# Kernel tuning notes

Hardware: AMD Instinct MI355X
Metric: run time of the kernel (lower is better)

The kernel has to match this reference:

```python
import jax, jax.numpy as jnp
import numpy as np

B, N, C, H, KHOP = 8, 1024, 512, 16, 2
HD = C // H
VALID = 768          # valid (non-padded) nodes per batch row
E = B * VALID * 32   # ~deg 32 per valid node
BN_EPS = 1e-5
LN_EPS = 1e-5


def setup_inputs() -> dict:
    key = jax.random.key(0)
    ks = jax.random.split(key, 12)
    x = jax.random.normal(ks[0], (B, N, C), jnp.float32)
    shift = jax.random.normal(ks[1], (B, C), jnp.float32) * 0.1
    scale = jax.random.normal(ks[2], (B, C), jnp.float32) * 0.1
    # fixed-size valid prefix per row -> static shapes under jit
    mask = jnp.broadcast_to(jnp.arange(N) < VALID, (B, N))
    # edges live inside a single graph (same batch row), only among valid nodes,
    # expressed directly in flattened [B*N] index space (== compacted indexing up to relabeling)
    eb = jax.random.randint(ks[3], (E,), 0, B)
    es = jax.random.randint(ks[4], (E,), 0, VALID)
    ed = jax.random.randint(ks[5], (E,), 0, VALID)
    edge_index = jnp.stack([eb * N + es, eb * N + ed]).astype(jnp.int32)
    w = lambda k, s: jax.random.normal(k, s, jnp.float32) * 0.02
    gin_eps = jnp.zeros((KHOP,), jnp.float32)
    gin_w1 = w(ks[6], (KHOP, C, 2 * C)); gin_b1 = jnp.zeros((KHOP, 2 * C), jnp.float32)
    gin_bn_g = jnp.ones((KHOP, 2 * C), jnp.float32); gin_bn_b = jnp.zeros((KHOP, 2 * C), jnp.float32)
    gin_w2 = w(ks[7], (KHOP, 2 * C, C)); gin_b2 = jnp.zeros((KHOP, C), jnp.float32)
    ln_g = jnp.ones((C,), jnp.float32); ln_b = jnp.zeros((C,), jnp.float32)
    qkv_w = w(ks[8], (C, 3 * C)); qkv_b = jnp.zeros((3 * C,), jnp.float32)
    proj_w = w(ks[9], (C, C)); proj_b = jnp.zeros((C,), jnp.float32)
    return dict(x=x, shift=shift, scale=scale, mask=mask, edge_index=edge_index,
                gin_eps=gin_eps, gin_w1=gin_w1, gin_b1=gin_b1, gin_bn_g=gin_bn_g,
                gin_bn_b=gin_bn_b, gin_w2=gin_w2, gin_b2=gin_b2, ln_g=ln_g, ln_b=ln_b,
                qkv_w=qkv_w, qkv_b=qkv_b, proj_w=proj_w, proj_b=proj_b)


def _gin_layer(h, mask_f, cnt, src, dst, eps, w1, b1, g, bt, w2, b2):
    # GINConv: mlp((1+eps)*x_i + sum_{j->i} x_j); MLP = Linear->BatchNorm(batch stats over valid nodes)->ReLU->Linear
    agg = jax.ops.segment_sum(h[src], dst, num_segments=B * N)  # scatter-add messages
    z = (1.0 + eps) * h + agg
    pre = z @ w1 + b1                              # [B*N, 2C]
    mw = mask_f[:, None]
    mean = (pre * mw).sum(0) / cnt                 # masked BN statistics (valid nodes only)
    var = (((pre - mean) ** 2) * mw).sum(0) / cnt  # biased var, as torch BatchNorm
    hn = jax.nn.relu(g * (pre - mean) * jax.lax.rsqrt(var + BN_EPS) + bt)
    return (hn @ w2 + b2) * mw                     # zero out padded nodes (x_struct stays 0 there)


def reference(x, shift, scale, mask, edge_index, gin_eps, gin_w1, gin_b1, gin_bn_g,
              gin_bn_b, gin_w2, gin_b2, ln_g, ln_b, qkv_w, qkv_b, proj_w, proj_b):
    xf = x.reshape(B * N, C)
    mask_f = mask.reshape(-1).astype(x.dtype)
    cnt = mask_f.sum()
    src, dst = edge_index[0], edge_index[1]
    # structure extractor: k-hop GIN with residual after the first hop
    h = _gin_layer(xf * mask_f[:, None], mask_f, cnt, src, dst, gin_eps[0],
                   gin_w1[0], gin_b1[0], gin_bn_g[0], gin_bn_b[0], gin_w2[0], gin_b2[0])
    for i in range(1, KHOP):
        h = _gin_layer(h, mask_f, cnt, src, dst, gin_eps[i],
                       gin_w1[i], gin_b1[i], gin_bn_g[i], gin_bn_b[i], gin_w2[i], gin_b2[i]) + h
    xs = x + h.reshape(B, N, C)  # x + x_struct (x_struct zero on padded nodes)
    # LayerNorm + modulate
    mu = xs.mean(-1, keepdims=True)
    va = xs.var(-1, keepdims=True)
    xn = (xs - mu) * jax.lax.rsqrt(va + LN_EPS) * ln_g + ln_b
    xm = xn * (1.0 + scale[:, None, :]) + shift[:, None, :]
    # SDPA attention with key padding mask
    qkv = (xm @ qkv_w + qkv_b).reshape(B, N, 3, H, HD).transpose(2, 0, 3, 1, 4)
    q, k, v = qkv[0], qkv[1], qkv[2]                       # [B,H,N,HD]
    scores = jnp.einsum('bhqd,bhkd->bhqk', q, k) * (HD ** -0.5)
    scores = scores + jnp.where(mask[:, None, None, :], 0.0, -1e9)
    attn = jax.nn.softmax(scores, axis=-1)
    out = jnp.einsum('bhqk,bhkd->bhqd', attn, v).transpose(0, 2, 1, 3).reshape(B, N, C)
    return out @ proj_w + proj_b
```

## Files before the change

### kernel.cpp

```cpp
#include <hip/hip_runtime.h>
#include <hip/hip_bf16.h>

constexpr int Bc    = 8;
constexpr int Nn    = 1024;
constexpr int Cc    = 512;
constexpr int Hh    = 16;
constexpr int HD    = 32;
constexpr int VALID = 768;
constexpr float CNT_INV = 1.0f / 6144.0f;
constexpr float BN_EPS = 1e-5f;
constexpr float LN_EPS = 1e-5f;
constexpr int ROWS = Bc * Nn;
constexpr int VROWS = Bc * VALID;

typedef short s16x8 __attribute__((ext_vector_type(8)));
typedef float f32x4 __attribute__((ext_vector_type(4)));

static __device__ __forceinline__ unsigned short f2bf(float f) {
    __hip_bfloat16 h = __float2bfloat16(f);
    return *reinterpret_cast<unsigned short*>(&h);
}
static __device__ __forceinline__ float bf2f(unsigned short u) {
    unsigned int v = (unsigned int)u << 16;
    union { unsigned int u; float f; } c; c.u = v;
    return c.f;
}

static __device__ __forceinline__ int vswz(int d) {
    return ((((d >> 3) ^ (d >> 1)) & 3) << 1) | (d & 1);
}

__global__ __launch_bounds__(256) void k_wt_all(const float* __restrict__ gw1,
                                                const float* __restrict__ gw2,
                                                const float* __restrict__ qkvw,
                                                const float* __restrict__ projw,
                                                const float* __restrict__ x,
                                                unsigned short* __restrict__ w1t,
                                                unsigned short* __restrict__ w2t,
                                                unsigned short* __restrict__ qkvt,
                                                unsigned short* __restrict__ projt,
                                                unsigned short* __restrict__ xb,
                                                float* __restrict__ stats,
                                                int* __restrict__ ideg) {
    const int bi = blockIdx.x;
    if (bi >= 3072) {
        int e = (bi - 3072) * 2048 + threadIdx.x * 8;
        float4 a = *(const float4*)&x[e];
        float4 b = *(const float4*)&x[e + 4];
        s16x8 o;
        o[0] = (short)f2bf(a.x); o[1] = (short)f2bf(a.y);
        o[2] = (short)f2bf(a.z); o[3] = (short)f2bf(a.w);
        o[4] = (short)f2bf(b.x); o[5] = (short)f2bf(b.y);
        o[6] = (short)f2bf(b.z); o[7] = (short)f2bf(b.w);
        *(s16x8*)&xb[e] = o;
        return;
    }
    if (bi == 0) {
        for (int i = threadIdx.x; i < 4096; i += 256) stats[i] = 0.f;
    } else if (bi == 1) {
        for (int i = threadIdx.x; i < 8192; i += 256) ideg[i] = 0;
    }

    const float* W; unsigned short* Wt; int K, N, bx, by;
    if (bi < 1024) {
        int z = bi >> 9, r = bi & 511;
        W = gw1 + (size_t)z * 524288; Wt = w1t + (size_t)z * 524288;
        K = 512; N = 1024; bx = r & 31; by = r >> 5;
    } else if (bi < 2048) {
        int z = (bi - 1024) >> 9, r = (bi - 1024) & 511;
        W = gw2 + (size_t)z * 524288; Wt = w2t + (size_t)z * 524288;
        K = 1024; N = 512; bx = r & 15; by = r >> 4;
    } else if (bi < 2816) {
        int r = bi - 2048;
        W = qkvw; Wt = qkvt; K = 512; N = 1536; bx = r % 48; by = r / 48;
    } else {
        int r = bi - 2816;
        W = projw; Wt = projt; K = 512; N = 512; bx = r & 15; by = r >> 4;
    }

    __shared__ float t[32][33];
    const int k0 = by * 32, n0 = bx * 32;
    int kk = threadIdx.x >> 3, nn = (threadIdx.x & 7) * 4;
    float4 v = *(const float4*)&W[(size_t)(k0 + kk) * N + n0 + nn];
    t[kk][nn] = v.x; t[kk][nn + 1] = v.y; t[kk][nn + 2] = v.z; t[kk][nn + 3] = v.w;
    __syncthreads();
    int nn2 = threadIdx.x >> 3, kk2 = (threadIdx.x & 7) * 4;
    ushort4 o;
    o.x = f2bf(t[kk2][nn2]);     o.y = f2bf(t[kk2 + 1][nn2]);
    o.z = f2bf(t[kk2 + 2][nn2]); o.w = f2bf(t[kk2 + 3][nn2]);
    *(ushort4*)&Wt[(size_t)(n0 + nn2) * K + k0 + kk2] = o;
}

__global__ __launch_bounds__(256) void k_count(const int* __restrict__ ei,
                                               int* __restrict__ deg, int E) {
    int e = blockIdx.x * 256 + threadIdx.x;
    if (e < E) atomicAdd(&deg[ei[E + e]], 1);
}

__global__ __launch_bounds__(1024) void k_scan(const int* __restrict__ deg,
                                               int* __restrict__ start,
                                               int* __restrict__ cursor) {
    __shared__ int csum[1024];
    const int t = threadIdx.x;
    const int base = t * 8;
    int local[8];
    int s = 0;
#pragma unroll
    for (int i = 0; i < 8; ++i) { local[i] = deg[base + i]; s += local[i]; }
    csum[t] = s;
    __syncthreads();
    for (int off = 1; off < 1024; off <<= 1) {
        int v = (t >= off) ? csum[t - off] : 0;
        __syncthreads();
        if (t >= off) csum[t] += v;
        __syncthreads();
    }
    int excl = (t == 0) ? 0 : csum[t - 1];
#pragma unroll
    for (int i = 0; i < 8; ++i) {
        start[base + i]  = excl;
        cursor[base + i] = excl;
        excl += local[i];
    }
    if (t == 1023) start[8192] = excl;
}

__global__ __launch_bounds__(256) void k_fill(const int* __restrict__ ei,
                                              int* __restrict__ cursor,
                                              int* __restrict__ list, int E) {
    int e = blockIdx.x * 256 + threadIdx.x;
    if (e < E) {
        int pos = atomicAdd(&cursor[ei[E + e]], 1);
        list[pos] = ei[e];
    }
}

__global__ __launch_bounds__(128) void k_gather_z(const unsigned short* __restrict__ h,
                                                  const int* __restrict__ start,
                                                  const int* __restrict__ list,
                                                  const float* __restrict__ epsArr,
                                                  int layer,
                                                  unsigned short* __restrict__ z) {
    const int vr = blockIdx.x;
    const int batch = vr / 768;
    const int row = batch * 1024 + (vr - batch * 768);
    const int c = threadIdx.x * 4;
    const int s0 = start[row], s1 = start[row + 1];
    const float e1 = 1.0f + epsArr[layer];
    const unsigned short* hp = h + c;
    ushort4 bv = *(const ushort4*)&h[(size_t)row * 512 + c];
    float a0 = bf2f(bv.x) * e1, a1 = bf2f(bv.y) * e1;
    float a2 = bf2f(bv.z) * e1, a3 = bf2f(bv.w) * e1;
    int j = s0;
    for (; j + 4 <= s1; j += 4) {
        int sA = list[j], sB = list[j + 1], sC = list[j + 2], sD = list[j + 3];
        ushort4 vA = *(const ushort4*)&hp[(size_t)sA * 512];
        ushort4 vB = *(const ushort4*)&hp[(size_t)sB * 512];
        ushort4 vC = *(const ushort4*)&hp[(size_t)sC * 512];
        ushort4 vD = *(const ushort4*)&hp[(size_t)sD * 512];
        a0 += bf2f(vA.x); a1 += bf2f(vA.y); a2 += bf2f(vA.z); a3 += bf2f(vA.w);
        a0 += bf2f(vB.x); a1 += bf2f(vB.y); a2 += bf2f(vB.z); a3 += bf2f(vB.w);
        a0 += bf2f(vC.x); a1 += bf2f(vC.y); a2 += bf2f(vC.z); a3 += bf2f(vC.w);
        a0 += bf2f(vD.x); a1 += bf2f(vD.y); a2 += bf2f(vD.z); a3 += bf2f(vD.w);
    }
    for (; j < s1; ++j) {
        int sA = list[j];
        ushort4 vA = *(const ushort4*)&hp[(size_t)sA * 512];
        a0 += bf2f(vA.x); a1 += bf2f(vA.y); a2 += bf2f(vA.z); a3 += bf2f(vA.w);
    }
    ushort4 o;
    o.x = f2bf(a0); o.y = f2bf(a1); o.z = f2bf(a2); o.w = f2bf(a3);
    *(ushort4*)&z[(size_t)row * 512 + c] = o;
}

template <bool RESIDUAL, bool STATS, bool SKIPM, bool OUTBF, bool QSCALE, bool HBF>
__global__ __launch_bounds__(256) void k_gemm_bf(const unsigned short* __restrict__ A,
                                                 const unsigned short* __restrict__ Bt,
                                                 const float* __restrict__ bias,
                                                 const float* __restrict__ res,
                                                 void* __restrict__ Cd,
                                                 float* __restrict__ stats,
                                                 unsigned short* __restrict__ hb,
                                                 int K, int Nc) {
    __shared__ unsigned short Al[128 * 64];
    __shared__ unsigned short Bl[128 * 64];
    const int tid  = threadIdx.x;
    const int by   = blockIdx.y;
    const int bm   = SKIPM ? ((by / 6) * 1024 + (by % 6) * 128) : (by * 128);
    const int bn   = blockIdx.x * 128;
    const int wid  = tid >> 6, lane = tid & 63;
    const int wr   = wid >> 1, wc = wid & 1;
    const int lo16 = lane & 15, g = lane >> 4;

    const int sr = tid >> 1;
    const int sh = tid & 1;
    const size_t a_off = (size_t)(bm + sr) * K + sh * 32;
    const size_t b_off = (size_t)(bn + sr) * K + sh * 32;

    f32x4 acc[4][4];
#pragma unroll
    for (int m = 0; m < 4; ++m)
#pragma unroll
        for (int n = 0; n < 4; ++n) acc[m][n] = (f32x4){0.f, 0.f, 0.f, 0.f};

    const int NT = K >> 6;
    s16x8 ar[4], br[4];
    {
        const s16x8* ap = (const s16x8*)(A + a_off);
        const s16x8* bp = (const s16x8*)(Bt + b_off);
#pragma unroll
        for (int i = 0; i < 4; ++i) { ar[i] = ap[i]; br[i] = bp[i]; }
    }

    for (int kt = 0; kt < NT; ++kt) {
        __syncthreads();
#pragma unroll
        for (int i = 0; i < 4; ++i) {
            int sl = (sh * 4 + i) ^ (sr & 7);
            *(s16x8*)&Al[sr * 64 + sl * 8] = ar[i];
            *(s16x8*)&Bl[sr * 64 + sl * 8] = br[i];
        }
        __syncthreads();
        if (kt + 1 < NT) {
            const s16x8* ap = (const s16x8*)(A + a_off + (size_t)(kt + 1) * 64);
            const s16x8* bp = (const s16x8*)(Bt + b_off + (size_t)(kt + 1) * 64);
#pragma unroll
            for (int i = 0; i < 4; ++i) { ar[i] = ap[i]; br[i] = bp[i]; }
        }
#pragma unroll
        for (int ks = 0; ks < 2; ++ks) {
            s16x8 af[4], bfr[4];
#pragma unroll
            for (int m = 0; m < 4; ++m) {
                int r = wr * 64 + m * 16 + lo16;
                int sl = (ks * 4 + g) ^ (r & 7);
                af[m] = *(const s16x8*)&Al[r * 64 + sl * 8];
            }
#pragma unroll
            for (int n = 0; n < 4; ++n) {
                int r = wc * 64 + n * 16 + lo16;
                int sl = (ks * 4 + g) ^ (r & 7);
                bfr[n] = *(const s16x8*)&Bl[r * 64 + sl * 8];
            }
            __builtin_amdgcn_s_setprio(1);
#pragma unroll
            for (int m = 0; m < 4; ++m)
#pragma unroll
                for (int n = 0; n < 4; ++n)
                    acc[m][n] = __builtin_amdgcn_mfma_f32_16x16x32_bf16(
                        af[m], bfr[n], acc[m][n], 0, 0, 0);
            __builtin_amdgcn_s_setprio(0);
        }
    }

#pragma unroll
    for (int n = 0; n < 4; ++n) {
        int col = bn + wc * 64 + n * 16 + lo16;
        float bb = bias[col];
        bool qs = QSCALE && (col < 512);
        float s = 0.f, s2 = 0.f;
#pragma unroll
        for (int m = 0; m < 4; ++m) {
#pragma unroll
            for (int ri = 0; ri < 4; ++ri) {
                int row = bm + wr * 64 + m * 16 + g * 4 + ri;
                float v = acc[m][n][ri] + bb;
                if (STATS) { s += v; s2 += v * v; }
                if (RESIDUAL) v += res[(size_t)row * Nc + col];
                if (QSCALE && qs) v *= 0.17677669529663687f;
                if (OUTBF) ((unsigned short*)Cd)[(size_t)row * Nc + col] = f2bf(v);
                else       ((float*)Cd)[(size_t)row * Nc + col] = v;
                if (HBF)   hb[(size_t)row * Nc + col] = f2bf(v);
            }
        }
        if (STATS) {
            s  += __shfl_xor(s, 16);  s  += __shfl_xor(s, 32);
            s2 += __shfl_xor(s2, 16); s2 += __shfl_xor(s2, 32);
            if (g == 0) {
                atomicAdd(&stats[col], s);
                atomicAdd(&stats[1024 + col], s2);
            }
        }
    }
}

__global__ __launch_bounds__(256) void k_bn_apply(const float* __restrict__ pre,
                                                  const float* __restrict__ stats,
                                                  const float* __restrict__ g,
                                                  const float* __restrict__ bt,
                                                  unsigned short* __restrict__ hn) {
    const int vr = blockIdx.x;
    const int batch = vr / 768;
    const int row = batch * 1024 + (vr - batch * 768);
    const int c0 = threadIdx.x * 4;
    const size_t off = (size_t)row * 1024 + c0;
    float4 v  = *(const float4*)&pre[off];
    float4 sm = *(const float4*)&stats[c0];
    float4 sq = *(const float4*)&stats[1024 + c0];
    float4 gv = *(const float4*)&g[c0];
    float4 bv = *(const float4*)&bt[c0];

    float m0 = sm.x * CNT_INV, m1 = sm.y * CNT_INV, m2 = sm.z * CNT_INV, m3 = sm.w * CNT_INV;
    float r0 = rsqrtf(sq.x * CNT_INV - m0 * m0 + BN_EPS);
    float r1 = rsqrtf(sq.y * CNT_INV - m1 * m1 + BN_EPS);
    float r2 = rsqrtf(sq.z * CNT_INV - m2 * m2 + BN_EPS);
    float r3 = rsqrtf(sq.w * CNT_INV - m3 * m3 + BN_EPS);
    ushort4 o;
    o.x = f2bf(fmaxf(gv.x * (v.x - m0) * r0 + bv.x, 0.f));
    o.y = f2bf(fmaxf(gv.y * (v.y - m1) * r1 + bv.y, 0.f));
    o.z = f2bf(fmaxf(gv.z * (v.z - m2) * r2 + bv.z, 0.f));
    o.w = f2bf(fmaxf(gv.w * (v.w - m3) * r3 + bv.w, 0.f));
    *(ushort4*)&hn[off] = o;
}

__global__ __launch_bounds__(256) void k_ln_mod(const float* __restrict__ x,
                                                const float* __restrict__ h,
                                                const float* __restrict__ lg,
                                                const float* __restrict__ lb,
                                                const float* __restrict__ sc,
                                                const float* __restrict__ sh,
                                                unsigned short* __restrict__ xm) {
    int row  = blockIdx.x * 4 + (threadIdx.x >> 6);
    int lane = threadIdx.x & 63;
    const size_t base = (size_t)row * 512 + lane * 8;
    const bool val = (row & 1023) < VALID;

    float v[8];
    float4 a0 = *(const float4*)&x[base],     a1 = *(const float4*)&x[base + 4];
    float4 b0 = *(const float4*)&h[base],     b1 = *(const float4*)&h[base + 4];
    if (!val) { b0.x=b0.y=b0.z=b0.w=0.f; b1.x=b1.y=b1.z=b1.w=0.f; }
    v[0] = a0.x + b0.x; v[1] = a0.y + b0.y; v[2] = a0.z + b0.z; v[3] = a0.w + b0.w;
    v[4] = a1.x + b1.x; v[5] = a1.y + b1.y; v[6] = a1.z + b1.z; v[7] = a1.w + b1.w;

    float s = 0.f, s2 = 0.f;
#pragma unroll
    for (int j = 0; j < 8; ++j) { s += v[j]; s2 += v[j] * v[j]; }
#pragma unroll
    for (int off = 32; off; off >>= 1) {
        s  += __shfl_xor(s, off);
        s2 += __shfl_xor(s2, off);
    }
    float mu  = s * (1.0f / 512.0f);
    float var = s2 * (1.0f / 512.0f) - mu * mu;
    float rs  = rsqrtf(var + LN_EPS);

    int c0 = lane * 8;
    int bidx = row >> 10;
    const float* scp = sc + (size_t)bidx * 512 + c0;
    const float* shp = sh + (size_t)bidx * 512 + c0;
    s16x8 o;
#pragma unroll
    for (int j = 0; j < 8; ++j) {
        float xn = (v[j] - mu) * rs * lg[c0 + j] + lb[c0 + j];
        o[j] = (short)f2bf(xn * (1.0f + scp[j]) + shp[j]);
    }
    *(s16x8*)&xm[base] = o;
}

__global__ __launch_bounds__(256) void k_attn_mfma(const unsigned short* __restrict__ qkv,
                                                   unsigned short* __restrict__ att) {
    __shared__ __align__(16) unsigned short Kl[128 * 32];
    __shared__ __align__(16) unsigned short Vt[32 * 128];
    __shared__ __align__(16) unsigned short Pl[4][16 * 128];

    const int w    = threadIdx.x >> 6;
    const int lane = threadIdx.x & 63;
    const int bh   = blockIdx.x;
    const int b    = bh >> 4, h = bh & 15;
    const int qt   = blockIdx.y;
    const int lo16 = lane & 15;
    const int g    = lane >> 4;

    const int qrow = qt * 64 + w * 16 + lo16;
    s16x8 qf = *(const s16x8*)&qkv[(size_t)(b * 1024 + qrow) * 1536 + h * 32 + g * 8];

    f32x4 o0 = {0.f, 0.f, 0.f, 0.f}, o1 = {0.f, 0.f, 0.f, 0.f};
    float l_run = 0.f;

    const size_t kvbase = (size_t)(b * 1024) * 1536 + h * 32;

    const int kr_r = threadIdx.x >> 2;
    const int kr_g = threadIdx.x & 3;
    const int vk0  = (threadIdx.x >> 2) * 2;
    const int vgg  = threadIdx.x & 3;

    s16x8 kA, kB, vA, vB;
    {
        const unsigned short* kp = &qkv[kvbase + (size_t)kr_r * 1536 + 512 + kr_g * 8];
        kA = *(const s16x8*)kp;
        kB = *(const s16x8*)(kp + (size_t)64 * 1536);
        const unsigned short* vp = &qkv[kvbase + (size_t)vk0 * 1536 + 1024 + vgg * 8];
        vA = *(const s16x8*)vp;
        vB = *(const s16x8*)(vp + 1536);
    }

    for (int kc = 0; kc < VALID; kc += 128) {
        __syncthreads();

        {
            int slot = kr_g ^ ((kr_r >> 1) & 3);
            *(s16x8*)&Kl[kr_r * 32 + slot * 8] = kA;
            int r2 = 64 + kr_r;
            slot = kr_g ^ ((r2 >> 1) & 3);
            *(s16x8*)&Kl[r2 * 32 + slot * 8] = kB;
        }
#pragma unroll
        for (int j = 0; j < 8; ++j) {
            int d = vgg * 8 + j;
            int slot = (vk0 >> 3) ^ vswz(d);
            int elem = d * 128 + slot * 8 + (vk0 & 7);
            unsigned int pack = (unsigned int)(unsigned short)vA[j] |
                                ((unsigned int)(unsigned short)vB[j] << 16);
            *(unsigned int*)&Vt[elem] = pack;
        }
        __syncthreads();

        if (kc + 128 < VALID) {
            const unsigned short* kp = &qkv[kvbase + (size_t)(kc + 128 + kr_r) * 1536 + 512 + kr_g * 8];
            kA = *(const s16x8*)kp;
            kB = *(const s16x8*)(kp + (size_t)64 * 1536);
            const unsigned short* vp = &qkv[kvbase + (size_t)(kc + 128 + vk0) * 1536 + 1024 + vgg * 8];
            vA = *(const s16x8*)vp;
            vB = *(const s16x8*)(vp + 1536);
        }

        f32x4 sc[8];
        __builtin_amdgcn_s_setprio(1);
#pragma unroll
        for (int t = 0; t < 8; ++t) {
            int r = t * 16 + lo16;
            int slot = g ^ ((r >> 1) & 3);
            s16x8 kf = *(const s16x8*)&Kl[r * 32 + slot * 8];
            f32x4 z = {0.f, 0.f, 0.f, 0.f};
            sc[t] = __builtin_amdgcn_mfma_f32_16x16x32_bf16(kf, qf, z, 0, 0, 0);
        }
        __builtin_amdgcn_s_setprio(0);

        float lsum = 0.f;
#pragma unroll
        for (int t = 0; t < 8; ++t) {
            float p0 = __expf(sc[t][0]);
            float p1 = __expf(sc[t][1]);
            float p2 = __expf(sc[t][2]);
            float p3 = __expf(sc[t][3]);
            lsum += (p0 + p1) + (p2 + p3);
            int kstart = t * 16 + g * 4;
            int slot = (kstart >> 3) ^ (lo16 & 7);
            int elem = lo16 * 128 + slot * 8 + (kstart & 7);
            unsigned int lo = (unsigned int)f2bf(p0) | ((unsigned int)f2bf(p1) << 16);
            unsigned int hi = (unsigned int)f2bf(p2) | ((unsigned int)f2bf(p3) << 16);
            uint2 pk; pk.x = lo; pk.y = hi;
            *(uint2*)&Pl[w][elem] = pk;
        }
        l_run += lsum;

        asm volatile("s_waitcnt lgkmcnt(0)" ::: "memory");
        __builtin_amdgcn_sched_barrier(0);

        __builtin_amdgcn_s_setprio(1);
#pragma unroll
        for (int sub = 0; sub < 4; ++sub) {
            int slotp = (sub * 4 + g) ^ (lo16 & 7);
            s16x8 pa = *(const s16x8*)&Pl[w][lo16 * 128 + slotp * 8];
            int d0 = lo16;
            s16x8 vb0 = *(const s16x8*)&Vt[d0 * 128 + (((sub * 4 + g) ^ vswz(d0)) * 8)];
            int d1 = 16 + lo16;
            s16x8 vb1 = *(const s16x8*)&Vt[d1 * 128 + (((sub * 4 + g) ^ vswz(d1)) * 8)];
            o0 = __builtin_amdgcn_mfma_f32_16x16x32_bf16(pa, vb0, o0, 0, 0, 0);
            o1 = __builtin_amdgcn_mfma_f32_16x16x32_bf16(pa, vb1, o1, 0, 0, 0);
        }
        __builtin_amdgcn_s_setprio(0);
    }

    l_run += __shfl_xor(l_run, 16);
    l_run += __shfl_xor(l_run, 32);
#pragma unroll
    for (int r = 0; r < 4; ++r) {
        float lr = __shfl(l_run, g * 4 + r);
        float inv = 1.f / lr;
        int qq = qt * 64 + w * 16 + g * 4 + r;
        unsigned short* op = att + ((size_t)(b * 1024 + qq) * 512 + h * 32);
        op[lo16]      = f2bf(o0[r] * inv);
        op[16 + lo16] = f2bf(o1[r] * inv);
    }
}

extern "C" void kernel_launch(void* const* d_in, const int* in_sizes, int n_in,
                              void* d_out, int out_size, void* d_ws, size_t ws_size,
                              hipStream_t stream) {
    const float* x     = (const float*)d_in[0];
    const float* shift = (const float*)d_in[1];
    const float* scale = (const float*)d_in[2];
    const int*   ei    = (const int*)d_in[4];
    const float* geps  = (const float*)d_in[5];
    const float* gw1   = (const float*)d_in[6];
    const float* gb1   = (const float*)d_in[7];
    const float* gbg   = (const float*)d_in[8];
    const float* gbb   = (const float*)d_in[9];
    const float* gw2   = (const float*)d_in[10];
    const float* gb2   = (const float*)d_in[11];
    const float* lng   = (const float*)d_in[12];
    const float* lnb   = (const float*)d_in[13];
    const float* qkvw  = (const float*)d_in[14];
    const float* qkvb  = (const float*)d_in[15];
    const float* projw = (const float*)d_in[16];
    const float* projb = (const float*)d_in[17];
    const int E = in_sizes[4] / 2;

    float* ws    = (float*)d_ws;
    float* bufA  = ws;
    float* bufB  = ws + 4194304;
    float* preq  = ws + 8388608;
    float* stats = ws + 20971520;
    int*   ideg    = (int*)(ws + 20975616);
    int*   istart  = ideg + 8192;
    int*   icursor = istart + 8193;
    int*   ilist   = icursor + 8192;
    unsigned short* hnb = (unsigned short*)(ws + 16777216);
    unsigned short* wts = (unsigned short*)(ws + 21200896);
    unsigned short* w1t   = wts;
    unsigned short* w2t   = wts + 1048576;
    unsigned short* qkvt  = wts + 2097152;
    unsigned short* projt = wts + 2883584;
    unsigned short* xb = (unsigned short*)preq;
    unsigned short* hb = (unsigned short*)(preq + 2097152);

    k_wt_all<<<5120, 256, 0, stream>>>(gw1, gw2, qkvw, projw, x,
                                       w1t, w2t, qkvt, projt, xb, stats, ideg);

    k_count<<<(E + 255) / 256, 256, 0, stream>>>(ei, ideg, E);
    k_scan<<<1, 1024, 0, stream>>>(ideg, istart, icursor);
    k_fill<<<(E + 255) / 256, 256, 0, stream>>>(ei, icursor, ilist, E);

    for (int layer = 0; layer < 2; ++layer) {
        const unsigned short* hin = layer ? hb : xb;
        unsigned short* zb = (unsigned short*)(layer ? bufA : bufB);
        float* st = stats + layer * 2048;
        k_gather_z<<<VROWS, 128, 0, stream>>>(hin, istart, ilist, geps, layer, zb);
        k_gemm_bf<false, true, true, false, false, false><<<dim3(8, 48), 256, 0, stream>>>(
            zb, w1t + (size_t)layer * 524288, gb1 + layer * 1024, nullptr,
            preq, st, nullptr, 512, 1024);
        k_bn_apply<<<VROWS, 256, 0, stream>>>(preq, st, gbg + layer * 1024,
                                              gbb + layer * 1024, hnb);
        if (layer == 0) {
            k_gemm_bf<false, false, true, false, false, true><<<dim3(4, 48), 256, 0, stream>>>(
                hnb, w2t, gb2, nullptr, bufB, nullptr, hb, 1024, 512);
        } else {
            k_gemm_bf<true, false, true, false, false, false><<<dim3(4, 48), 256, 0, stream>>>(
                hnb, w2t + 524288, gb2 + 512, bufB, bufA, nullptr, nullptr, 1024, 512);
        }
    }

    unsigned short* xmb = (unsigned short*)bufB;
    k_ln_mod<<<2048, 256, 0, stream>>>(x, bufA, lng, lnb, scale, shift, xmb);
    unsigned short* qkvb16 = (unsigned short*)preq;
    k_gemm_bf<false, false, false, true, true, false><<<dim3(12, 64), 256, 0, stream>>>(
        xmb, qkvt, qkvb, nullptr, qkvb16, nullptr, nullptr, 512, 1536);
    unsigned short* attb = (unsigned short*)bufA;
    k_attn_mfma<<<dim3(128, 16), 256, 0, stream>>>(qkvb16, attb);
    k_gemm_bf<false, false, false, false, false, false><<<dim3(4, 64), 256, 0, stream>>>(
        attb, projt, projb, nullptr, (float*)d_out, nullptr, nullptr, 512, 512);
}
```

Measured before the change: 235.7 us.

## Widen gather/BN vectors, store GIN preactivations in bf16, skip padded KV, double query tiles

Several changes at once. The gather and BN-apply kernels move to 8-wide bf16 vectors with half the threads per block. The first GIN GEMM now writes its pre-activations as bf16 instead of fp32, which cuts traffic into BN-apply but loses precision before normalisation. The QKV GEMM skips the K/V columns for padded rows. Attention processes two 64-row query tiles per block, halving the grid and reusing each loaded K/V tile, and replaces __expf with a raw v_exp_f32 by folding log2(e) into the Q scale.

```diff
diff --git a/kernel.cpp b/kernel.cpp
--- a/kernel.cpp
+++ b/kernel.cpp
@@ -12,6 +12,7 @@
 constexpr float LN_EPS = 1e-5f;
 constexpr int ROWS = Bc * Nn;
 constexpr int VROWS = Bc * VALID;
+constexpr float QSCL = 0.25500526764086547f;
 
 typedef short s16x8 __attribute__((ext_vector_type(8)));
 typedef float f32x4 __attribute__((ext_vector_type(4)));
@@ -21,9 +22,11 @@
     return *reinterpret_cast<unsigned short*>(&h);
 }
 static __device__ __forceinline__ float bf2f(unsigned short u) {
-    unsigned int v = (unsigned int)u << 16;
-    union { unsigned int u; float f; } c; c.u = v;
+    union { unsigned int u; float f; } c; c.u = (unsigned int)u << 16;
     return c.f;
+}
+static __device__ __forceinline__ float exp2_fast(float x) {
+    float r; asm("v_exp_f32 %0, %1" : "=v"(r) : "v"(x)); return r;
 }
 
 static __device__ __forceinline__ int vswz(int d) {
@@ -135,45 +138,51 @@
     }
 }
 
-__global__ __launch_bounds__(128) void k_gather_z(const unsigned short* __restrict__ h,
-                                                  const int* __restrict__ start,
-                                                  const int* __restrict__ list,
-                                                  const float* __restrict__ epsArr,
-                                                  int layer,
-                                                  unsigned short* __restrict__ z) {
+__global__ __launch_bounds__(64) void k_gather_z(const unsigned short* __restrict__ h,
+                                                 const int* __restrict__ start,
+                                                 const int* __restrict__ list,
+                                                 const float* __restrict__ epsArr,
+                                                 int layer,
+                                                 unsigned short* __restrict__ z) {
     const int vr = blockIdx.x;
     const int batch = vr / 768;
     const int row = batch * 1024 + (vr - batch * 768);
-    const int c = threadIdx.x * 4;
+    const int c = threadIdx.x * 8;
     const int s0 = start[row], s1 = start[row + 1];
     const float e1 = 1.0f + epsArr[layer];
     const unsigned short* hp = h + c;
-    ushort4 bv = *(const ushort4*)&h[(size_t)row * 512 + c];
-    float a0 = bf2f(bv.x) * e1, a1 = bf2f(bv.y) * e1;
-    float a2 = bf2f(bv.z) * e1, a3 = bf2f(bv.w) * e1;
+    s16x8 bv = *(const s16x8*)&h[(size_t)row * 512 + c];
+    float a[8];
+#pragma unroll
+    for (int i = 0; i < 8; ++i) a[i] = bf2f((unsigned short)bv[i]) * e1;
     int j = s0;
     for (; j + 4 <= s1; j += 4) {
         int sA = list[j], sB = list[j + 1], sC = list[j + 2], sD = list[j + 3];
-        ushort4 vA = *(const ushort4*)&hp[(size_t)sA * 512];
-        ushort4 vB = *(const ushort4*)&hp[(size_t)sB * 512];
-        ushort4 vC = *(const ushort4*)&hp[(size_t)sC * 512];
-        ushort4 vD = *(const ushort4*)&hp[(size_t)sD * 512];
-        a0 += bf2f(vA.x); a1 += bf2f(vA.y); a2 += bf2f(vA.z); a3 += bf2f(vA.w);
-        a0 += bf2f(vB.x); a1 += bf2f(vB.y); a2 += bf2f(vB.z); a3 += bf2f(vB.w);
-        a0 += bf2f(vC.x); a1 += bf2f(vC.y); a2 += bf2f(vC.z); a3 += bf2f(vC.w);
-        a0 += bf2f(vD.x); a1 += bf2f(vD.y); a2 += bf2f(vD.z); a3 += bf2f(vD.w);
+        s16x8 vA = *(const s16x8*)&hp[(size_t)sA * 512];
+        s16x8 vB = *(const s16x8*)&hp[(size_t)sB * 512];
+        s16x8 vC = *(const s16x8*)&hp[(size_t)sC * 512];
+        s16x8 vD = *(const s16x8*)&hp[(size_t)sD * 512];
+#pragma unroll
+        for (int i = 0; i < 8; ++i) {
+            a[i] += bf2f((unsigned short)vA[i]);
+            a[i] += bf2f((unsigned short)vB[i]);
+            a[i] += bf2f((unsigned short)vC[i]);
+            a[i] += bf2f((unsigned short)vD[i]);
+        }
     }
     for (; j < s1; ++j) {
-        int sA = list[j];
-        ushort4 vA = *(const ushort4*)&hp[(size_t)sA * 512];
-        a0 += bf2f(vA.x); a1 += bf2f(vA.y); a2 += bf2f(vA.z); a3 += bf2f(vA.w);
-    }
-    ushort4 o;
-    o.x = f2bf(a0); o.y = f2bf(a1); o.z = f2bf(a2); o.w = f2bf(a3);
-    *(ushort4*)&z[(size_t)row * 512 + c] = o;
-}
-
-template <bool RESIDUAL, bool STATS, bool SKIPM, bool OUTBF, bool QSCALE, bool HBF>
+        s16x8 vA = *(const s16x8*)&hp[(size_t)list[j] * 512];
+#pragma unroll
+        for (int i = 0; i < 8; ++i) a[i] += bf2f((unsigned short)vA[i]);
+    }
+    s16x8 o;
+#pragma unroll
+    for (int i = 0; i < 8; ++i) o[i] = (short)f2bf(a[i]);
+    *(s16x8*)&z[(size_t)row * 512 + c] = o;
+}
+
+template <bool RESIDUAL, bool STATS, bool SKIPM, bool OUTBF, bool QSCALE,
+          bool HBF, bool SKIPKV>
 __global__ __launch_bounds__(256) void k_gemm_bf(const unsigned short* __restrict__ A,
                                                  const unsigned short* __restrict__ Bt,
                                                  const float* __restrict__ bias,
@@ -188,6 +197,7 @@
     const int by   = blockIdx.y;
     const int bm   = SKIPM ? ((by / 6) * 1024 + (by % 6) * 128) : (by * 128);
     const int bn   = blockIdx.x * 128;
+    if (SKIPKV && (by & 7) >= 6 && bn >= 512) return;
     const int wid  = tid >> 6, lane = tid & 63;
     const int wr   = wid >> 1, wc = wid & 1;
     const int lo16 = lane & 15, g = lane >> 4;
@@ -267,7 +277,7 @@
                 float v = acc[m][n][ri] + bb;
                 if (STATS) { s += v; s2 += v * v; }
                 if (RESIDUAL) v += res[(size_t)row * Nc + col];
-                if (QSCALE && qs) v *= 0.17677669529663687f;
+                if (QSCALE && qs) v *= QSCL;
                 if (OUTBF) ((unsigned short*)Cd)[(size_t)row * Nc + col] = f2bf(v);
                 else       ((float*)Cd)[(size_t)row * Nc + col] = v;
                 if (HBF)   hb[(size_t)row * Nc + col] = f2bf(v);
@@ -284,7 +294,7 @@
     }
 }
 
-__global__ __launch_bounds__(256) void k_bn_apply(const float* __restrict__ pre,
+__global__ __launch_bounds__(128) void k_bn_apply(const unsigned short* __restrict__ pre,
                                                   const float* __restrict__ stats,
                                                   const float* __restrict__ g,
                                                   const float* __restrict__ bt,
@@ -292,25 +302,19 @@
     const int vr = blockIdx.x;
     const int batch = vr / 768;
     const int row = batch * 1024 + (vr - batch * 768);
-    const int c0 = threadIdx.x * 4;
+    const int c0 = threadIdx.x * 8;
     const size_t off = (size_t)row * 1024 + c0;
-    float4 v  = *(const float4*)&pre[off];
-    float4 sm = *(const float4*)&stats[c0];
-    float4 sq = *(const float4*)&stats[1024 + c0];
-    float4 gv = *(const float4*)&g[c0];
-    float4 bv = *(const float4*)&bt[c0];
-
-    float m0 = sm.x * CNT_INV, m1 = sm.y * CNT_INV, m2 = sm.z * CNT_INV, m3 = sm.w * CNT_INV;
-    float r0 = rsqrtf(sq.x * CNT_INV - m0 * m0 + BN_EPS);
-    float r1 = rsqrtf(sq.y * CNT_INV - m1 * m1 + BN_EPS);
-    float r2 = rsqrtf(sq.z * CNT_INV - m2 * m2 + BN_EPS);
-    float r3 = rsqrtf(sq.w * CNT_INV - m3 * m3 + BN_EPS);
-    ushort4 o;
-    o.x = f2bf(fmaxf(gv.x * (v.x - m0) * r0 + bv.x, 0.f));
-    o.y = f2bf(fmaxf(gv.y * (v.y - m1) * r1 + bv.y, 0.f));
-    o.z = f2bf(fmaxf(gv.z * (v.z - m2) * r2 + bv.z, 0.f));
-    o.w = f2bf(fmaxf(gv.w * (v.w - m3) * r3 + bv.w, 0.f));
-    *(ushort4*)&hn[off] = o;
+    s16x8 v = *(const s16x8*)&pre[off];
+    s16x8 o;
+#pragma unroll
+    for (int i = 0; i < 8; ++i) {
+        float sm = stats[c0 + i], sq = stats[1024 + c0 + i];
+        float m = sm * CNT_INV;
+        float r = rsqrtf(sq * CNT_INV - m * m + BN_EPS);
+        float hv = g[c0 + i] * (bf2f((unsigned short)v[i]) - m) * r + bt[c0 + i];
+        o[i] = (short)f2bf(fmaxf(hv, 0.f));
+    }
+    *(s16x8*)&hn[off] = o;
 }
 
 __global__ __launch_bounds__(256) void k_ln_mod(const float* __restrict__ x,
@@ -371,11 +375,16 @@
     const int lo16 = lane & 15;
     const int g    = lane >> 4;
 
-    const int qrow = qt * 64 + w * 16 + lo16;
-    s16x8 qf = *(const s16x8*)&qkv[(size_t)(b * 1024 + qrow) * 1536 + h * 32 + g * 8];
-
-    f32x4 o0 = {0.f, 0.f, 0.f, 0.f}, o1 = {0.f, 0.f, 0.f, 0.f};
-    float l_run = 0.f;
+    s16x8 qf[2];
+#pragma unroll
+    for (int qi = 0; qi < 2; ++qi) {
+        int qrow = qt * 128 + qi * 64 + w * 16 + lo16;
+        qf[qi] = *(const s16x8*)&qkv[(size_t)(b * 1024 + qrow) * 1536 + h * 32 + g * 8];
+    }
+
+    f32x4 o0[2] = {{0.f,0.f,0.f,0.f},{0.f,0.f,0.f,0.f}};
+    f32x4 o1[2] = {{0.f,0.f,0.f,0.f},{0.f,0.f,0.f,0.f}};
+    float l_run[2] = {0.f, 0.f};
 
     const size_t kvbase = (size_t)(b * 1024) * 1536 + h * 32;
 
@@ -424,64 +433,71 @@
             vB = *(const s16x8*)(vp + 1536);
         }
 
-        f32x4 sc[8];
-        __builtin_amdgcn_s_setprio(1);
-#pragma unroll
-        for (int t = 0; t < 8; ++t) {
-            int r = t * 16 + lo16;
-            int slot = g ^ ((r >> 1) & 3);
-            s16x8 kf = *(const s16x8*)&Kl[r * 32 + slot * 8];
-            f32x4 z = {0.f, 0.f, 0.f, 0.f};
-            sc[t] = __builtin_amdgcn_mfma_f32_16x16x32_bf16(kf, qf, z, 0, 0, 0);
-        }
-        __builtin_amdgcn_s_setprio(0);
-
-        float lsum = 0.f;
-#pragma unroll
-        for (int t = 0; t < 8; ++t) {
-            float p0 = __expf(sc[t][0]);
-            float p1 = __expf(sc[t][1]);
-            float p2 = __expf(sc[t][2]);
-            float p3 = __expf(sc[t][3]);
-            lsum += (p0 + p1) + (p2 + p3);
-            int kstart = t * 16 + g * 4;
-            int slot = (kstart >> 3) ^ (lo16 & 7);
-            int elem = lo16 * 128 + slot * 8 + (kstart & 7);
-            unsigned int lo = (unsigned int)f2bf(p0) | ((unsigned int)f2bf(p1) << 16);
-            unsigned int hi = (unsigned int)f2bf(p2) | ((unsigned int)f2bf(p3) << 16);
-            uint2 pk; pk.x = lo; pk.y = hi;
-            *(uint2*)&Pl[w][elem] = pk;
-        }
-        l_run += lsum;
-
-        asm volatile("s_waitcnt lgkmcnt(0)" ::: "memory");
-        __builtin_amdgcn_sched_barrier(0);
-
-        __builtin_amdgcn_s_setprio(1);
-#pragma unroll
-        for (int sub = 0; sub < 4; ++sub) {
-            int slotp = (sub * 4 + g) ^ (lo16 & 7);
-            s16x8 pa = *(const s16x8*)&Pl[w][lo16 * 128 + slotp * 8];
-            int d0 = lo16;
-            s16x8 vb0 = *(const s16x8*)&Vt[d0 * 128 + (((sub * 4 + g) ^ vswz(d0)) * 8)];
-            int d1 = 16 + lo16;
-            s16x8 vb1 = *(const s16x8*)&Vt[d1 * 128 + (((sub * 4 + g) ^ vswz(d1)) * 8)];
-            o0 = __builtin_amdgcn_mfma_f32_16x16x32_bf16(pa, vb0, o0, 0, 0, 0);
-            o1 = __builtin_amdgcn_mfma_f32_16x16x32_bf16(pa, vb1, o1, 0, 0, 0);
-        }
-        __builtin_amdgcn_s_setprio(0);
-    }
-
-    l_run += __shfl_xor(l_run, 16);
-    l_run += __shfl_xor(l_run, 32);
-#pragma unroll
-    for (int r = 0; r < 4; ++r) {
-        float lr = __shfl(l_run, g * 4 + r);
-        float inv = 1.f / lr;
-        int qq = qt * 64 + w * 16 + g * 4 + r;
-        unsigned short* op = att + ((size_t)(b * 1024 + qq) * 512 + h * 32);
-        op[lo16]      = f2bf(o0[r] * inv);
-        op[16 + lo16] = f2bf(o1[r] * inv);
+#pragma unroll
+        for (int qi = 0; qi < 2; ++qi) {
+            f32x4 sc[8];
+            __builtin_amdgcn_s_setprio(1);
+#pragma unroll
+            for (int t = 0; t < 8; ++t) {
+                int r = t * 16 + lo16;
+                int slot = g ^ ((r >> 1) & 3);
+                s16x8 kf = *(const s16x8*)&Kl[r * 32 + slot * 8];
+                f32x4 z = {0.f, 0.f, 0.f, 0.f};
+                sc[t] = __builtin_amdgcn_mfma_f32_16x16x32_bf16(kf, qf[qi], z, 0, 0, 0);
+            }
+            __builtin_amdgcn_s_setprio(0);
+
+            float lsum = 0.f;
+#pragma unroll
+            for (int t = 0; t < 8; ++t) {
+                float p0 = exp2_fast(sc[t][0]);
+                float p1 = exp2_fast(sc[t][1]);
+                float p2 = exp2_fast(sc[t][2]);
+                float p3 = exp2_fast(sc[t][3]);
+                lsum += (p0 + p1) + (p2 + p3);
+                int kstart = t * 16 + g * 4;
+                int slot = (kstart >> 3) ^ (lo16 & 7);
+                int elem = lo16 * 128 + slot * 8 + (kstart & 7);
+                unsigned int lo = (unsigned int)f2bf(p0) | ((unsigned int)f2bf(p1) << 16);
+                unsigned int hi = (unsigned int)f2bf(p2) | ((unsigned int)f2bf(p3) << 16);
+                uint2 pk; pk.x = lo; pk.y = hi;
+                *(uint2*)&Pl[w][elem] = pk;
+            }
+            l_run[qi] += lsum;
+
+            asm volatile("s_waitcnt lgkmcnt(0)" ::: "memory");
+            __builtin_amdgcn_sched_barrier(0);
+
+            __builtin_amdgcn_s_setprio(1);
+#pragma unroll
+            for (int sub = 0; sub < 4; ++sub) {
+                int slotp = (sub * 4 + g) ^ (lo16 & 7);
+                s16x8 pa = *(const s16x8*)&Pl[w][lo16 * 128 + slotp * 8];
+                int d0 = lo16;
+                s16x8 vb0 = *(const s16x8*)&Vt[d0 * 128 + (((sub * 4 + g) ^ vswz(d0)) * 8)];
+                int d1 = 16 + lo16;
+                s16x8 vb1 = *(const s16x8*)&Vt[d1 * 128 + (((sub * 4 + g) ^ vswz(d1)) * 8)];
+                o0[qi] = __builtin_amdgcn_mfma_f32_16x16x32_bf16(pa, vb0, o0[qi], 0, 0, 0);
+                o1[qi] = __builtin_amdgcn_mfma_f32_16x16x32_bf16(pa, vb1, o1[qi], 0, 0, 0);
+            }
+            __builtin_amdgcn_s_setprio(0);
+        }
+    }
+
+#pragma unroll
+    for (int qi = 0; qi < 2; ++qi) {
+        float l = l_run[qi];
+        l += __shfl_xor(l, 16);
+        l += __shfl_xor(l, 32);
+#pragma unroll
+        for (int r = 0; r < 4; ++r) {
+            float lr = __shfl(l, g * 4 + r);
+            float inv = 1.f / lr;
+            int qq = qt * 128 + qi * 64 + w * 16 + g * 4 + r;
+            unsigned short* op = att + ((size_t)(b * 1024 + qq) * 512 + h * 32);
+            op[lo16]      = f2bf(o0[qi][r] * inv);
+            op[16 + lo16] = f2bf(o1[qi][r] * inv);
+        }
     }
 }
 
@@ -522,8 +538,9 @@
     unsigned short* w2t   = wts + 1048576;
     unsigned short* qkvt  = wts + 2097152;
     unsigned short* projt = wts + 2883584;
-    unsigned short* xb = (unsigned short*)preq;
-    unsigned short* hb = (unsigned short*)(preq + 2097152);
+    unsigned short* xb  = (unsigned short*)preq;
+    unsigned short* hb  = (unsigned short*)(preq + 2097152);
+    unsigned short* pre = (unsigned short*)preq;
 
     k_wt_all<<<5120, 256, 0, stream>>>(gw1, gw2, qkvw, projw, x,
                                        w1t, w2t, qkvt, projt, xb, stats, ideg);
@@ -536,17 +553,20 @@
         const unsigned short* hin = layer ? hb : xb;
         unsigned short* zb = (unsigned short*)(layer ? bufA : bufB);
         float* st = stats + layer * 2048;
-        k_gather_z<<<VROWS, 128, 0, stream>>>(hin, istart, ilist, geps, layer, zb);
-        k_gemm_bf<false, true, true, false, false, false><<<dim3(8, 48), 256, 0, stream>>>(
+        k_gather_z<<<VROWS, 64, 0, stream>>>(hin, istart, ilist, geps, layer, zb);
+        k_gemm_bf<false, true, true, true, false, false, false>
+            <<<dim3(8, 48), 256, 0, stream>>>(
             zb, w1t + (size_t)layer * 524288, gb1 + layer * 1024, nullptr,
-            preq, st, nullptr, 512, 1024);
-        k_bn_apply<<<VROWS, 256, 0, stream>>>(preq, st, gbg + layer * 1024,
+            pre, st, nullptr, 512, 1024);
+        k_bn_apply<<<VROWS, 128, 0, stream>>>(pre, st, gbg + layer * 1024,
                                               gbb + layer * 1024, hnb);
         if (layer == 0) {
-            k_gemm_bf<false, false, true, false, false, true><<<dim3(4, 48), 256, 0, stream>>>(
+            k_gemm_bf<false, false, true, false, false, true, false>
+                <<<dim3(4, 48), 256, 0, stream>>>(
                 hnb, w2t, gb2, nullptr, bufB, nullptr, hb, 1024, 512);
         } else {
-            k_gemm_bf<true, false, true, false, false, false><<<dim3(4, 48), 256, 0, stream>>>(
+            k_gemm_bf<true, false, true, false, false, false, false>
+                <<<dim3(4, 48), 256, 0, stream>>>(
                 hnb, w2t + 524288, gb2 + 512, bufB, bufA, nullptr, nullptr, 1024, 512);
         }
     }
@@ -554,10 +574,12 @@
     unsigned short* xmb = (unsigned short*)bufB;
     k_ln_mod<<<2048, 256, 0, stream>>>(x, bufA, lng, lnb, scale, shift, xmb);
     unsigned short* qkvb16 = (unsigned short*)preq;
-    k_gemm_bf<false, false, false, true, true, false><<<dim3(12, 64), 256, 0, stream>>>(
+    k_gemm_bf<false, false, false, true, true, false, true>
+        <<<dim3(12, 64), 256, 0, stream>>>(
         xmb, qkvt, qkvb, nullptr, qkvb16, nullptr, nullptr, 512, 1536);
     unsigned short* attb = (unsigned short*)bufA;
-    k_attn_mfma<<<dim3(128, 16), 256, 0, stream>>>(qkvb16, attb);
-    k_gemm_bf<false, false, false, false, false, false><<<dim3(4, 64), 256, 0, stream>>>(
+    k_attn_mfma<<<dim3(128, 8), 256, 0, stream>>>(qkvb16, attb);
+    k_gemm_bf<false, false, false, false, false, false, false>
+        <<<dim3(4, 64), 256, 0, stream>>>(
         attb, projt, projb, nullptr, (float*)d_out, nullptr, nullptr, 512, 512);
 }
```

New measurement: 231.8 us. About the same (-1.7%).
